# Kernel tuning notes

Hardware: AMD Instinct MI355X
Metric: run time of the kernel (lower is better)

The kernel has to match this reference:

```python
import jax, jax.numpy as jnp
import numpy as np

N = 10000
E = 640000
F = 128      # in_dim
H = 4        # heads
Dh = 32      # head_dim = ceil(128/4)
INNER = H * Dh   # 128 == out_dim -> W_out is Identity
OUT = 128
SCALE = 1.0 / np.sqrt(float(Dh))
LN_EPS = 1e-5


def setup_inputs() -> dict:
    key = jax.random.key(0)
    ks = jax.random.split(key, 8)
    s = 1.0 / np.sqrt(F)
    nodes = jax.random.normal(ks[0], (N, F), dtype=jnp.float32)
    edge_index = jax.random.randint(ks[1], (2, E), 0, N, dtype=jnp.int32)
    W_Q = jax.random.uniform(ks[2], (F, INNER), jnp.float32, -s, s)
    W_K = jax.random.uniform(ks[3], (F, INNER), jnp.float32, -s, s)
    W_V = jax.random.uniform(ks[4], (F, INNER), jnp.float32, -s, s)
    W_res = jax.random.uniform(ks[5], (F, OUT), jnp.float32, -s, s)
    b_res = jax.random.uniform(ks[6], (OUT,), jnp.float32, -s, s)
    gamma = jnp.ones((OUT,), jnp.float32)
    beta = jnp.zeros((OUT,), jnp.float32)
    return {"nodes": nodes, "W_Q": W_Q, "W_K": W_K, "W_V": W_V,
            "W_res": W_res, "b_res": b_res, "gamma": gamma, "beta": beta,
            "edge_index": edge_index}


def reference(nodes, W_Q, W_K, W_V, W_res, b_res, gamma, beta, edge_index):
    n = nodes.shape[0]
    src = edge_index[0]
    dst = edge_index[1]
    # node-level projections, split into heads: [N, H, Dh]
    Q = (nodes @ W_Q).reshape(n, H, Dh)
    K = (nodes @ W_K).reshape(n, H, Dh)
    V = (nodes @ W_V).reshape(n, H, Dh)
    # per-edge gathers: q from dst, k/v from src
    q = Q[dst]          # [E, H, Dh]
    k = K[src]
    v = V[src]
    score = jnp.sum(q * k, axis=-1) * SCALE      # [E, H]
    # segment softmax over dst
    mx = jax.ops.segment_max(score, dst, num_segments=n)   # [N, H]
    mx = jnp.where(jnp.isfinite(mx), mx, 0.0)               # guard empty segments
    ex = jnp.exp(score - mx[dst])                           # [E, H]
    sm = jax.ops.segment_sum(ex, dst, num_segments=n)       # [N, H]
    alpha = ex / (sm[dst] + 1e-12)                          # [E, H]
    # scatter-aggregate weighted values
    agg = jax.ops.segment_sum(alpha[:, :, None] * v, dst, num_segments=n)  # [N, H, Dh]
    H_cat = agg.reshape(n, INNER)                # W_out is Identity (inner == out)
    H_out = H_cat + nodes @ W_res + b_res        # residual projection
    # LayerNorm(out_dim)
    mu = jnp.mean(H_out, axis=-1, keepdims=True)
    var = jnp.mean(jnp.square(H_out - mu), axis=-1, keepdims=True)
    x_hat = (H_out - mu) * jax.lax.rsqrt(var + LN_EPS)
    return gamma * x_hat + beta
```

## Files before the change

kernel.cpp:

```cpp
#include <hip/hip_runtime.h>
#include <math.h>

#define FDIM 128
#define NP 32
#define NMAX 10240
static constexpr float SC2 = 0.17677669529663687f * 1.4426950408889634f;
static constexpr float LN_EPS = 1e-5f;

typedef __attribute__((ext_vector_type(8))) short bf16x8;
typedef __attribute__((ext_vector_type(4))) float f32x4;

__device__ __forceinline__ unsigned short f2bf(float f) {
    unsigned u = __float_as_uint(f);
    unsigned r = u + 0x7FFFu + ((u >> 16) & 1u);
    return (unsigned short)(r >> 16);
}

__global__ __launch_bounds__(256) void prep_kernel(
    const float* __restrict__ nodes,
    const float* __restrict__ Wq, const float* __restrict__ Wk,
    const float* __restrict__ Wv, const float* __restrict__ Wr,
    unsigned short* __restrict__ nodesb, unsigned short* __restrict__ Wt, int N)
{
    const int tid = threadIdx.x;
    const int b = blockIdx.x;
    if (b < 640) {
        const int idx = b * 2048 + tid * 8;
        if (idx < N * FDIM) {
            const float4 f0 = *reinterpret_cast<const float4*>(&nodes[idx]);
            const float4 f1 = *reinterpret_cast<const float4*>(&nodes[idx + 4]);
            ushort4 o0, o1;
            o0.x = f2bf(f0.x); o0.y = f2bf(f0.y); o0.z = f2bf(f0.z); o0.w = f2bf(f0.w);
            o1.x = f2bf(f1.x); o1.y = f2bf(f1.y); o1.z = f2bf(f1.z); o1.w = f2bf(f1.w);
            *reinterpret_cast<ushort4*>(&nodesb[idx]) = o0;
            *reinterpret_cast<ushort4*>(&nodesb[idx + 4]) = o1;
        }
    } else {
        const int t = b - 640;
        const int wiW = t >> 2, q = t & 3;
        const float* __restrict__ W = (wiW == 0) ? Wq : (wiW == 1) ? Wk : (wiW == 2) ? Wv : Wr;
        const int c = q * 32 + (tid >> 3);
        const int k0 = (tid & 7) * 16;
        unsigned short* dp = &Wt[(size_t)wiW * 16384 + c * 128 + k0];
        #pragma unroll
        for (int kk = 0; kk < 16; ++kk)
            dp[kk] = f2bf(W[(k0 + kk) * FDIM + c]);
    }
}

__global__ __launch_bounds__(256) void gemm_hist_kernel(
    const unsigned short* __restrict__ nodesb,
    const unsigned short* __restrict__ Wt,
    const float* __restrict__ br,
    unsigned short* __restrict__ Qu, unsigned short* __restrict__ KVu,
    float* __restrict__ Rb, int N,
    const int* __restrict__ dst, int* __restrict__ bh, int E, int C)
{
    __shared__ __align__(16) char smem[52224];
    const int tid = threadIdx.x;
    const int wi = blockIdx.y;

    if (wi == 0) {
        const int p = blockIdx.x;
        if (p >= NP) return;
        int* h = (int*)smem;
        for (int i = tid; i < N; i += 256) h[i] = 0;
        __syncthreads();
        const int lo = p * C;
        const int hi = min(lo + C, E);
        const int n = hi - lo;
        if (n > 0) {
            if (((lo | E) & 3) == 0) {
                const int4* d4 = (const int4*)(dst + lo);
                const int n4 = n >> 2;
                for (int i = tid; i < n4; i += 256) {
                    int4 d = d4[i];
                    atomicAdd(&h[d.x], 1); atomicAdd(&h[d.y], 1);
                    atomicAdd(&h[d.z], 1); atomicAdd(&h[d.w], 1);
                }
                for (int i = lo + (n4 << 2) + tid; i < hi; i += 256)
                    atomicAdd(&h[dst[i]], 1);
            } else {
                for (int i = lo + tid; i < hi; i += 256)
                    atomicAdd(&h[dst[i]], 1);
            }
        }
        __syncthreads();
        for (int i = tid; i < N; i += 256) bh[p * N + i] = h[i];
        return;
    }

    const int gw = wi - 1;
    const int row0 = blockIdx.x * 64;
    unsigned short (*As)[136] = (unsigned short(*)[136])smem;
    unsigned short (*Ws)[136] = (unsigned short(*)[136])(smem + 64 * 272);

    #pragma unroll
    for (int i = 0; i < 4; ++i) {
        const int idx = tid + i * 256;
        const int r = idx >> 4, ch = idx & 15;
        const int gr = row0 + r;
        uint4 v = make_uint4(0u, 0u, 0u, 0u);
        if (gr < N) v = *reinterpret_cast<const uint4*>(&nodesb[(size_t)gr * 128 + ch * 8]);
        *reinterpret_cast<uint4*>(&As[r][ch * 8]) = v;
    }
    const unsigned short* Wg = &Wt[(size_t)gw * 16384];
    #pragma unroll
    for (int i = 0; i < 8; ++i) {
        const int idx = tid + i * 256;
        const int r = idx >> 4, ch = idx & 15;
        const uint4 v = *reinterpret_cast<const uint4*>(&Wg[r * 128 + ch * 8]);
        *reinterpret_cast<uint4*>(&Ws[r][ch * 8]) = v;
    }
    __syncthreads();

    const int w = tid >> 6;
    const int l = tid & 63;
    const int lr = l & 15;
    const int lh = l >> 4;

    f32x4 acc[8];
    #pragma unroll
    for (int ct = 0; ct < 8; ++ct) acc[ct] = (f32x4){0.f, 0.f, 0.f, 0.f};

    #pragma unroll
    for (int kc = 0; kc < 4; ++kc) {
        const bf16x8 a = *reinterpret_cast<const bf16x8*>(&As[w * 16 + lr][kc * 32 + lh * 8]);
        #pragma unroll
        for (int ct = 0; ct < 8; ++ct) {
            const bf16x8 bb = *reinterpret_cast<const bf16x8*>(&Ws[ct * 16 + lr][kc * 32 + lh * 8]);
            acc[ct] = __builtin_amdgcn_mfma_f32_16x16x32_bf16(a, bb, acc[ct], 0, 0, 0);
        }
    }

    const int rbase = row0 + w * 16 + lh * 4;
    #pragma unroll
    for (int ct = 0; ct < 8; ++ct) {
        const int col = ct * 16 + lr;
        float bc = 0.f;
        if (gw == 3) bc = br[col];
        #pragma unroll
        for (int r = 0; r < 4; ++r) {
            const int row = rbase + r;
            if (row >= N) continue;
            const float val = acc[ct][r];
            if (gw == 0)      Qu[(size_t)row * 128 + col] = f2bf(val);
            else if (gw == 1) KVu[(size_t)row * 256 + col] = f2bf(val);
            else if (gw == 2) KVu[(size_t)row * 256 + 128 + col] = f2bf(val);
            else              Rb[(size_t)row * 128 + col] = val + bc;
        }
    }
}

__global__ __launch_bounds__(256) void deg_kernel(
    const int* __restrict__ bh, int* __restrict__ deg, int N)
{
    const int d = blockIdx.x * 256 + threadIdx.x;
    if (d < N) {
        int s = 0;
        #pragma unroll
        for (int p = 0; p < NP; ++p) s += bh[p * N + d];
        deg[d] = s;
    }
}

__global__ __launch_bounds__(1024) void scan_kernel(
    const int* __restrict__ deg, int* __restrict__ rowptr, int N)
{
    __shared__ int tot[NMAX];
    __shared__ int csum[1024];
    const int tid = threadIdx.x;

    for (int d = tid; d < N; d += 1024) tot[d] = deg[d];
    __syncthreads();

    const int CH = (N + 1023) / 1024;
    const int b = tid * CH;
    const int e = min(b + CH, N);
    int s = 0;
    for (int i = b; i < e; ++i) s += tot[i];
    csum[tid] = s;
    __syncthreads();
    for (int off = 1; off < 1024; off <<= 1) {
        int t = (tid >= off) ? csum[tid - off] : 0;
        __syncthreads();
        csum[tid] += t;
        __syncthreads();
    }
    int run = csum[tid] - s;
    for (int i = b; i < e; ++i) {
        const int t = tot[i];
        rowptr[i] = run;
        run += t;
    }
    if (tid == 1023) rowptr[N] = csum[1023];
}

__global__ __launch_bounds__(256) void base_kernel(
    int* __restrict__ bh, const int* __restrict__ rowptr, int N)
{
    const int d = blockIdx.x * 256 + threadIdx.x;
    if (d < N) {
        int c = rowptr[d];
        #pragma unroll
        for (int p = 0; p < NP; ++p) {
            const int cnt = bh[p * N + d];
            bh[p * N + d] = c;
            c += cnt;
        }
    }
}

__global__ __launch_bounds__(256) void scatter_kernel(
    const int* __restrict__ src, const int* __restrict__ dst,
    const int* __restrict__ base, int* __restrict__ ssrc,
    int N, int E, int C)
{
    __shared__ int cur[NMAX];
    const int p = blockIdx.x, tid = threadIdx.x;
    for (int d = tid; d < N; d += 256) cur[d] = base[p * N + d];
    __syncthreads();

    const int lo = p * C;
    const int hi = min(lo + C, E);
    const int n = hi - lo;
    if (n <= 0) return;

    if (((lo | E) & 3) == 0) {
        const int4* s4 = (const int4*)(src + lo);
        const int4* d4 = (const int4*)(dst + lo);
        const int n4 = n >> 2;
        for (int i = tid; i < n4; i += 256) {
            int4 s = s4[i];
            int4 d = d4[i];
            int p0 = atomicAdd(&cur[d.x], 1); ssrc[p0] = s.x;
            int p1 = atomicAdd(&cur[d.y], 1); ssrc[p1] = s.y;
            int p2 = atomicAdd(&cur[d.z], 1); ssrc[p2] = s.z;
            int p3 = atomicAdd(&cur[d.w], 1); ssrc[p3] = s.w;
        }
        for (int i = lo + (n4 << 2) + tid; i < hi; i += 256) {
            int pos = atomicAdd(&cur[dst[i]], 1); ssrc[pos] = src[i];
        }
    } else {
        for (int i = lo + tid; i < hi; i += 256) {
            int pos = atomicAdd(&cur[dst[i]], 1); ssrc[pos] = src[i];
        }
    }
}

__global__ __launch_bounds__(256) void agg_kernel(
    const unsigned short* __restrict__ Qu, const unsigned short* __restrict__ KVu,
    const float* __restrict__ Rb,
    const int* __restrict__ rowptr, const int* __restrict__ ssrc,
    const float* __restrict__ gamma, const float* __restrict__ beta,
    float* __restrict__ out, int N)
{
    const int wave = threadIdx.x >> 6;
    const int lane = threadIdx.x & 63;
    const int qtr = lane >> 4;
    const int lq = lane & 15;
    const int n = blockIdx.x * 16 + wave * 4 + qtr;
    if (n >= N) return;
    const int d0 = lq * 8;

    const uint4 qu = *reinterpret_cast<const uint4*>(&Qu[(size_t)n * 128 + d0]);
    const float qf0 = __uint_as_float(qu.x << 16), qf1 = __uint_as_float(qu.x & 0xFFFF0000u);
    const float qf2 = __uint_as_float(qu.y << 16), qf3 = __uint_as_float(qu.y & 0xFFFF0000u);
    const float qf4 = __uint_as_float(qu.z << 16), qf5 = __uint_as_float(qu.z & 0xFFFF0000u);
    const float qf6 = __uint_as_float(qu.w << 16), qf7 = __uint_as_float(qu.w & 0xFFFF0000u);

    const int beg = rowptr[n];
    const int end = rowptr[n + 1];

    float4 A0a = make_float4(0.f, 0.f, 0.f, 0.f), A0b = A0a;
    float4 A1a = A0a, A1b = A0a, A2a = A0a, A2b = A0a, A3a = A0a, A3b = A0a;
    float L0 = 0.f, L1 = 0.f, L2 = 0.f, L3 = 0.f;

#define GATHER(S, NK, NV)                                                     \
    {                                                                         \
        const unsigned short* bp = &KVu[(size_t)(S) * 256 + d0];              \
        NK = *reinterpret_cast<const uint4*>(bp);                             \
        NV = *reinterpret_cast<const uint4*>(bp + 128);                       \
    }
#define STEP(KU, VU, Aa, Ab, L)                                               \
    {                                                                         \
        const float k0 = __uint_as_float((KU).x << 16), k1 = __uint_as_float((KU).x & 0xFFFF0000u); \
        const float k2 = __uint_as_float((KU).y << 16), k3 = __uint_as_float((KU).y & 0xFFFF0000u); \
        const float k4 = __uint_as_float((KU).z << 16), k5 = __uint_as_float((KU).z & 0xFFFF0000u); \
        const float k6 = __uint_as_float((KU).w << 16), k7 = __uint_as_float((KU).w & 0xFFFF0000u); \
        float p = qf0 * k0 + qf1 * k1 + qf2 * k2 + qf3 * k3                   \
                + qf4 * k4 + qf5 * k5 + qf6 * k6 + qf7 * k7;                  \
        p += __shfl_xor(p, 1);                                                \
        p += __shfl_xor(p, 2);                                                \
        const float e1 = exp2f(p * SC2);                                      \
        const float v0 = __uint_as_float((VU).x << 16), v1 = __uint_as_float((VU).x & 0xFFFF0000u); \
        const float v2 = __uint_as_float((VU).y << 16), v3 = __uint_as_float((VU).y & 0xFFFF0000u); \
        const float v4 = __uint_as_float((VU).z << 16), v5 = __uint_as_float((VU).z & 0xFFFF0000u); \
        const float v6 = __uint_as_float((VU).w << 16), v7 = __uint_as_float((VU).w & 0xFFFF0000u); \
        Aa.x += e1 * v0; Aa.y += e1 * v1; Aa.z += e1 * v2; Aa.w += e1 * v3;   \
        Ab.x += e1 * v4; Ab.y += e1 * v5; Ab.z += e1 * v6; Ab.w += e1 * v7;   \
        L += e1;                                                              \
    }

    uint4 nk0, nv0, nk1, nv1, nk2, nv2, nk3, nv3;
    int j = beg;
    const int nb = (end - beg) >> 2;
    if (nb > 0) {
        int c0i = ssrc[j], c1i = ssrc[j + 1], c2i = ssrc[j + 2], c3i = ssrc[j + 3];
        GATHER(c0i, nk0, nv0); GATHER(c1i, nk1, nv1);
        GATHER(c2i, nk2, nv2); GATHER(c3i, nk3, nv3);
        int x0 = ssrc[j + 4], x1 = ssrc[j + 5], x2 = ssrc[j + 6], x3 = ssrc[j + 7];
        for (int bi = 1; bi < nb; ++bi) {
            const uint4 ck0 = nk0, cv0 = nv0, ck1 = nk1, cv1 = nv1;
            const uint4 ck2 = nk2, cv2 = nv2, ck3 = nk3, cv3 = nv3;
            c0i = x0; c1i = x1; c2i = x2; c3i = x3;
            const int nbase = j + (bi + 1) * 4;
            x0 = ssrc[nbase]; x1 = ssrc[nbase + 1];
            x2 = ssrc[nbase + 2]; x3 = ssrc[nbase + 3];
            GATHER(c0i, nk0, nv0); GATHER(c1i, nk1, nv1);
            GATHER(c2i, nk2, nv2); GATHER(c3i, nk3, nv3);
            STEP(ck0, cv0, A0a, A0b, L0);
            STEP(ck1, cv1, A1a, A1b, L1);
            STEP(ck2, cv2, A2a, A2b, L2);
            STEP(ck3, cv3, A3a, A3b, L3);
        }
        STEP(nk0, nv0, A0a, A0b, L0);
        STEP(nk1, nv1, A1a, A1b, L1);
        STEP(nk2, nv2, A2a, A2b, L2);
        STEP(nk3, nv3, A3a, A3b, L3);
        j = beg + nb * 4;
    }
    for (; j < end; ++j) {
        const int s0 = ssrc[j];
        uint4 k0u, v0u;
        GATHER(s0, k0u, v0u);
        STEP(k0u, v0u, A0a, A0b, L0);
    }
#undef GATHER
#undef STEP

    const float L = (L0 + L1) + (L2 + L3);
    const float inv = 1.f / (L + 1e-12f);
    const float4 ra = *reinterpret_cast<const float4*>(&Rb[(size_t)n * 128 + d0]);
    const float4 rb = *reinterpret_cast<const float4*>(&Rb[(size_t)n * 128 + d0 + 4]);
    float xa0 = ((A0a.x + A1a.x) + (A2a.x + A3a.x)) * inv + ra.x;
    float xa1 = ((A0a.y + A1a.y) + (A2a.y + A3a.y)) * inv + ra.y;
    float xa2 = ((A0a.z + A1a.z) + (A2a.z + A3a.z)) * inv + ra.z;
    float xa3 = ((A0a.w + A1a.w) + (A2a.w + A3a.w)) * inv + ra.w;
    float xb0 = ((A0b.x + A1b.x) + (A2b.x + A3b.x)) * inv + rb.x;
    float xb1 = ((A0b.y + A1b.y) + (A2b.y + A3b.y)) * inv + rb.y;
    float xb2 = ((A0b.z + A1b.z) + (A2b.z + A3b.z)) * inv + rb.z;
    float xb3 = ((A0b.w + A1b.w) + (A2b.w + A3b.w)) * inv + rb.w;

    float s1v = (xa0 + xa1 + xa2 + xa3) + (xb0 + xb1 + xb2 + xb3);
    float s2v = xa0 * xa0 + xa1 * xa1 + xa2 * xa2 + xa3 * xa3
              + xb0 * xb0 + xb1 * xb1 + xb2 * xb2 + xb3 * xb3;
    #pragma unroll
    for (int off = 8; off; off >>= 1) {
        s1v += __shfl_xor(s1v, off);
        s2v += __shfl_xor(s2v, off);
    }
    const float mu = s1v * (1.f / 128.f);
    float var = s2v * (1.f / 128.f) - mu * mu;
    var = fmaxf(var, 0.f);
    const float rs = rsqrtf(var + LN_EPS);

    const float4 ga = *reinterpret_cast<const float4*>(&gamma[d0]);
    const float4 gb = *reinterpret_cast<const float4*>(&gamma[d0 + 4]);
    const float4 ba = *reinterpret_cast<const float4*>(&beta[d0]);
    const float4 bb = *reinterpret_cast<const float4*>(&beta[d0 + 4]);
    float4 oa, ob;
    oa.x = ga.x * (xa0 - mu) * rs + ba.x;
    oa.y = ga.y * (xa1 - mu) * rs + ba.y;
    oa.z = ga.z * (xa2 - mu) * rs + ba.z;
    oa.w = ga.w * (xa3 - mu) * rs + ba.w;
    ob.x = gb.x * (xb0 - mu) * rs + bb.x;
    ob.y = gb.y * (xb1 - mu) * rs + bb.y;
    ob.z = gb.z * (xb2 - mu) * rs + bb.z;
    ob.w = gb.w * (xb3 - mu) * rs + bb.w;
    *reinterpret_cast<float4*>(&out[(size_t)n * 128 + d0]) = oa;
    *reinterpret_cast<float4*>(&out[(size_t)n * 128 + d0 + 4]) = ob;
}

extern "C" void kernel_launch(void* const* d_in, const int* in_sizes, int n_in,
                              void* d_out, int out_size, void* d_ws, size_t ws_size,
                              hipStream_t stream)
{
    const float* nodes = (const float*)d_in[0];
    const float* W_Q   = (const float*)d_in[1];
    const float* W_K   = (const float*)d_in[2];
    const float* W_V   = (const float*)d_in[3];
    const float* W_res = (const float*)d_in[4];
    const float* b_res = (const float*)d_in[5];
    const float* gamma = (const float*)d_in[6];
    const float* beta  = (const float*)d_in[7];
    const int*   eidx  = (const int*)d_in[8];

    const int N = in_sizes[0] / FDIM;
    const int E = in_sizes[8] / 2;
    const int* src = eidx;
    const int* dst = eidx + E;

    float* out = (float*)d_out;

    unsigned short* KVu    = (unsigned short*)d_ws;
    unsigned short* Qu     = KVu + (size_t)N * 256;
    unsigned short* nodesb = Qu + (size_t)N * 128;
    unsigned short* Wt     = nodesb + (size_t)N * 128;
    float* Rb   = (float*)(Wt + 4 * 16384);
    int* bh     = (int*)(Rb + (size_t)N * 128);
    int* rowptr = bh + (size_t)NP * N;
    int* deg    = rowptr + (N + 1);
    int* ssrc   = deg + N;

    const int C = (((E + NP - 1) / NP) + 3) & ~3;
    const int nG = (N + 63) / 64;
    const int nB = (N + 255) / 256;

    prep_kernel<<<656, 256, 0, stream>>>(nodes, W_Q, W_K, W_V, W_res, nodesb, Wt, N);

    dim3 ggrid(nG, 5);
    gemm_hist_kernel<<<ggrid, 256, 0, stream>>>(nodesb, Wt, b_res,
                                                Qu, KVu, Rb, N, dst, bh, E, C);
    deg_kernel<<<nB, 256, 0, stream>>>(bh, deg, N);
    scan_kernel<<<1, 1024, 0, stream>>>(deg, rowptr, N);
    base_kernel<<<nB, 256, 0, stream>>>(bh, rowptr, N);
    scatter_kernel<<<NP, 256, 0, stream>>>(src, dst, bh, ssrc, N, E, C);
    agg_kernel<<<(N + 15) / 16, 256, 0, stream>>>(Qu, KVu, Rb, rowptr, ssrc,
                                                  gamma, beta, out, N);
}
```

Baseline: 100.4 us.

## Fuse bf16 node conversion into GEMM, use shuffle scan, double histogram partitions

```diff
diff --git a/kernel.cpp b/kernel.cpp
--- a/kernel.cpp
+++ b/kernel.cpp
@@ -2,7 +2,7 @@
 #include <math.h>
 
 #define FDIM 128
-#define NP 32
+#define NP 64
 #define NMAX 10240
 static constexpr float SC2 = 0.17677669529663687f * 1.4426950408889634f;
 static constexpr float LN_EPS = 1e-5f;
@@ -17,39 +17,24 @@
 }
 
 __global__ __launch_bounds__(256) void prep_kernel(
-    const float* __restrict__ nodes,
     const float* __restrict__ Wq, const float* __restrict__ Wk,
     const float* __restrict__ Wv, const float* __restrict__ Wr,
-    unsigned short* __restrict__ nodesb, unsigned short* __restrict__ Wt, int N)
+    unsigned short* __restrict__ Wt)
 {
     const int tid = threadIdx.x;
-    const int b = blockIdx.x;
-    if (b < 640) {
-        const int idx = b * 2048 + tid * 8;
-        if (idx < N * FDIM) {
-            const float4 f0 = *reinterpret_cast<const float4*>(&nodes[idx]);
-            const float4 f1 = *reinterpret_cast<const float4*>(&nodes[idx + 4]);
-            ushort4 o0, o1;
-            o0.x = f2bf(f0.x); o0.y = f2bf(f0.y); o0.z = f2bf(f0.z); o0.w = f2bf(f0.w);
-            o1.x = f2bf(f1.x); o1.y = f2bf(f1.y); o1.z = f2bf(f1.z); o1.w = f2bf(f1.w);
-            *reinterpret_cast<ushort4*>(&nodesb[idx]) = o0;
-            *reinterpret_cast<ushort4*>(&nodesb[idx + 4]) = o1;
-        }
-    } else {
-        const int t = b - 640;
-        const int wiW = t >> 2, q = t & 3;
-        const float* __restrict__ W = (wiW == 0) ? Wq : (wiW == 1) ? Wk : (wiW == 2) ? Wv : Wr;
-        const int c = q * 32 + (tid >> 3);
-        const int k0 = (tid & 7) * 16;
-        unsigned short* dp = &Wt[(size_t)wiW * 16384 + c * 128 + k0];
-        #pragma unroll
-        for (int kk = 0; kk < 16; ++kk)
-            dp[kk] = f2bf(W[(k0 + kk) * FDIM + c]);
-    }
+    const int t = blockIdx.x;
+    const int wiW = t >> 2, q = t & 3;
+    const float* __restrict__ W = (wiW == 0) ? Wq : (wiW == 1) ? Wk : (wiW == 2) ? Wv : Wr;
+    const int c = q * 32 + (tid >> 3);
+    const int k0 = (tid & 7) * 16;
+    unsigned short* dp = &Wt[(size_t)wiW * 16384 + c * 128 + k0];
+    #pragma unroll
+    for (int kk = 0; kk < 16; ++kk)
+        dp[kk] = f2bf(W[(k0 + kk) * FDIM + c]);
 }
 
 __global__ __launch_bounds__(256) void gemm_hist_kernel(
-    const unsigned short* __restrict__ nodesb,
+    const float* __restrict__ nodes,
     const unsigned short* __restrict__ Wt,
     const float* __restrict__ br,
     unsigned short* __restrict__ Qu, unsigned short* __restrict__ KVu,
@@ -96,13 +81,15 @@
     unsigned short (*Ws)[136] = (unsigned short(*)[136])(smem + 64 * 272);
 
     #pragma unroll
-    for (int i = 0; i < 4; ++i) {
+    for (int i = 0; i < 8; ++i) {
         const int idx = tid + i * 256;
-        const int r = idx >> 4, ch = idx & 15;
+        const int r = idx >> 5, c4 = idx & 31;
         const int gr = row0 + r;
-        uint4 v = make_uint4(0u, 0u, 0u, 0u);
-        if (gr < N) v = *reinterpret_cast<const uint4*>(&nodesb[(size_t)gr * 128 + ch * 8]);
-        *reinterpret_cast<uint4*>(&As[r][ch * 8]) = v;
+        float4 v = make_float4(0.f, 0.f, 0.f, 0.f);
+        if (gr < N) v = *reinterpret_cast<const float4*>(&nodes[(size_t)gr * FDIM + c4 * 4]);
+        ushort4 o;
+        o.x = f2bf(v.x); o.y = f2bf(v.y); o.z = f2bf(v.z); o.w = f2bf(v.w);
+        *reinterpret_cast<ushort4*>(&As[r][c4 * 4]) = o;
     }
     const unsigned short* Wg = &Wt[(size_t)gw * 16384];
     #pragma unroll
@@ -168,8 +155,10 @@
     const int* __restrict__ deg, int* __restrict__ rowptr, int N)
 {
     __shared__ int tot[NMAX];
-    __shared__ int csum[1024];
+    __shared__ int wsum[16];
     const int tid = threadIdx.x;
+    const int lane = tid & 63;
+    const int wid = tid >> 6;
 
     for (int d = tid; d < N; d += 1024) tot[d] = deg[d];
     __syncthreads();
@@ -179,21 +168,33 @@
     const int e = min(b + CH, N);
     int s = 0;
     for (int i = b; i < e; ++i) s += tot[i];
-    csum[tid] = s;
+
+    int incl = s;
+    #pragma unroll
+    for (int off = 1; off < 64; off <<= 1) {
+        int t = __shfl_up(incl, off);
+        if (lane >= off) incl += t;
+    }
+    if (lane == 63) wsum[wid] = incl;
     __syncthreads();
-    for (int off = 1; off < 1024; off <<= 1) {
-        int t = (tid >= off) ? csum[tid - off] : 0;
-        __syncthreads();
-        csum[tid] += t;
-        __syncthreads();
-    }
-    int run = csum[tid] - s;
+    if (wid == 0) {
+        int v = (lane < 16) ? wsum[lane] : 0;
+        #pragma unroll
+        for (int off = 1; off < 16; off <<= 1) {
+            int t = __shfl_up(v, off);
+            if (lane >= off) v += t;
+        }
+        if (lane < 16) wsum[lane] = v;
+    }
+    __syncthreads();
+    const int wbase = (wid > 0) ? wsum[wid - 1] : 0;
+    int run = wbase + incl - s;
     for (int i = b; i < e; ++i) {
         const int t = tot[i];
         rowptr[i] = run;
         run += t;
     }
-    if (tid == 1023) rowptr[N] = csum[1023];
+    if (tid == 1023) rowptr[N] = wsum[15];
 }
 
 __global__ __launch_bounds__(256) void base_kernel(
@@ -403,10 +404,9 @@
 
     float* out = (float*)d_out;
 
-    unsigned short* KVu    = (unsigned short*)d_ws;
-    unsigned short* Qu     = KVu + (size_t)N * 256;
-    unsigned short* nodesb = Qu + (size_t)N * 128;
-    unsigned short* Wt     = nodesb + (size_t)N * 128;
+    unsigned short* KVu = (unsigned short*)d_ws;
+    unsigned short* Qu  = KVu + (size_t)N * 256;
+    unsigned short* Wt  = Qu + (size_t)N * 128;
     float* Rb   = (float*)(Wt + 4 * 16384);
     int* bh     = (int*)(Rb + (size_t)N * 128);
     int* rowptr = bh + (size_t)NP * N;
@@ -417,10 +417,10 @@
     const int nG = (N + 63) / 64;
     const int nB = (N + 255) / 256;
 
-    prep_kernel<<<656, 256, 0, stream>>>(nodes, W_Q, W_K, W_V, W_res, nodesb, Wt, N);
+    prep_kernel<<<16, 256, 0, stream>>>(W_Q, W_K, W_V, W_res, Wt);
 
     dim3 ggrid(nG, 5);
-    gemm_hist_kernel<<<ggrid, 256, 0, stream>>>(nodesb, Wt, b_res,
+    gemm_hist_kernel<<<ggrid, 256, 0, stream>>>(nodes, Wt, b_res,
                                                 Qu, KVu, Rb, N, dst, bh, E, C);
     deg_kernel<<<nB, 256, 0, stream>>>(bh, deg, N);
     scan_kernel<<<1, 1024, 0, stream>>>(deg, rowptr, N);
```

Measured after the change: 95.28 us. 5.1% less time.
